# Performance work log

Measured on AMD Instinct MI355X. Metric: run time of the kernel, lower is better.

Reference implementation:

```python
import jax, jax.numpy as jnp
import numpy as np

L, B, F, H, C = 1024, 8, 256, 8, 32  # seq, batch, feature_dim, heads, head_size
EPS = 1e-5


def setup_inputs() -> dict:
    key = jax.random.key(0)
    ks = jax.random.split(key, 12)
    s = 0.02
    f32 = jnp.float32
    return {
        "features": jax.random.normal(ks[0], (L, B, F), f32),
        "ln_g": jnp.ones((F,), f32),
        "ln_b": jnp.zeros((F,), f32),
        "Wq": jax.random.normal(ks[1], (F, H * C), f32) * s,
        "bq": jnp.zeros((H * C,), f32),
        "Wk": jax.random.normal(ks[2], (F, H * C), f32) * s,
        "bk": jnp.zeros((H * C,), f32),
        "Wv": jax.random.normal(ks[3], (F, H * C), f32) * s,
        "bv": jnp.zeros((H * C,), f32),
        "Wb": jax.random.normal(ks[4], (F, H), f32) * s,
        "bb": jnp.zeros((H,), f32),
        "Wg": jax.random.normal(ks[5], (F, H * C), f32) * s,
        "bg": jnp.zeros((H * C,), f32),
        "Wo": jax.random.normal(ks[6], (H * C, F), f32) * s,
        "bo": jnp.zeros((F,), f32),
    }


def _layernorm(x, g, b):
    mu = jnp.mean(x, axis=-1, keepdims=True)
    var = jnp.var(x, axis=-1, keepdims=True)
    return (x - mu) * jax.lax.rsqrt(var + EPS) * g + b


def reference(features, ln_g, ln_b, Wq, bq, Wk, bk, Wv, bv, Wb, bb, Wg, bg, Wo, bo):
    # features: (L, B, F) -- sequence-first layout (see einsum axis analysis)
    x = _layernorm(features, ln_g, ln_b)
    q = (x @ Wq + bq).reshape(L, B, H, C)  # (Lq, B, H, C)
    k = (x @ Wk + bk).reshape(L, B, H, C)  # (Lk, B, H, C)
    v = (x @ Wv + bv).reshape(L, B, H, C)
    bias = x @ Wb + bb                      # (Lk, B, H) per-key-position bias
    gate = jax.nn.sigmoid(x @ Wg + bg).reshape(L, B, H, C)

    sq_c = 1.0 / np.sqrt(C).astype(np.float32)
    # logits[q, b, k, h]
    logits = jnp.einsum('qbhc,kbhc->qbkh', q, k) * sq_c
    logits = logits + jnp.transpose(bias, (1, 0, 2))[None]  # (1, B, Lk, H)
    w = jax.nn.softmax(logits, axis=2)                      # softmax over keys
    attn = jnp.einsum('qbkh,kbhc->qbhc', w, v)              # (Lq, B, H, C)
    out = (attn * gate).reshape(L, B, H * C)
    return out @ Wo + bo                                    # (L, B, F)
```

## Files before the change

kernel.cpp:

```cpp
#include <hip/hip_runtime.h>
#include <math.h>

#define LQ 1024
#define BB 8
#define FF 256
#define HH 8
#define CC 32
#define MROWS (LQ*BB)
static constexpr float EPSV  = 1e-5f;
static constexpr float LOG2E = 1.4426950408889634f;
static constexpr float C1    = 0.17677669529663687f * 1.4426950408889634f;

typedef short  short8  __attribute__((ext_vector_type(8)));
typedef short  short4v __attribute__((ext_vector_type(4)));
typedef float  float4v __attribute__((ext_vector_type(4)));

__device__ inline unsigned short f2bf(float f) {
    unsigned int u = __builtin_bit_cast(unsigned int, f);
    u += 0x7FFFu + ((u >> 16) & 1u);
    return (unsigned short)(u >> 16);
}
__device__ inline float bf2f(unsigned short h) {
    unsigned int u = ((unsigned int)h) << 16;
    return __builtin_bit_cast(float, u);
}
__device__ inline unsigned int cvt_pk_bf16(float a, float b) {
    unsigned int r;
    asm("v_cvt_pk_bf16_f32 %0, %1, %2" : "=v"(r) : "v"(a), "v"(b));
    return r;
}
__device__ __forceinline__ void gl_lds16(const unsigned short* g, unsigned short* l) {
    __builtin_amdgcn_global_load_lds(
        (const __attribute__((address_space(1))) void*)g,
        (__attribute__((address_space(3))) void*)l, 16, 0, 0);
}

__global__ __launch_bounds__(256)
void prep_ln_kernel(const float* __restrict__ x, const float* __restrict__ g,
                    const float* __restrict__ bln,
                    const float* __restrict__ Wq, const float* __restrict__ Wk,
                    const float* __restrict__ Wv, const float* __restrict__ Wg,
                    const float* __restrict__ Wo, const float* __restrict__ Wb,
                    const float* __restrict__ bq, const float* __restrict__ bk,
                    const float* __restrict__ bv, const float* __restrict__ bg,
                    unsigned short* __restrict__ xb, unsigned short* __restrict__ wt,
                    unsigned short* __restrict__ wto,
                    float* __restrict__ bcomb, float* __restrict__ wbt) {
    int bid = blockIdx.x;
    if (bid < 2048) {
        int wid  = threadIdx.x >> 6;
        int lane = threadIdx.x & 63;
        int row  = bid * 4 + wid;
        float4 v = reinterpret_cast<const float4*>(x + (size_t)row * FF)[lane];
        float s  = v.x + v.y + v.z + v.w;
        float sq = v.x*v.x + v.y*v.y + v.z*v.z + v.w*v.w;
        #pragma unroll
        for (int m = 1; m < 64; m <<= 1) {
            s  += __shfl_xor(s,  m);
            sq += __shfl_xor(sq, m);
        }
        float mean = s * (1.0f / FF);
        float var  = sq * (1.0f / FF) - mean * mean;
        float rstd = rsqrtf(var + EPSV);
        float4 gg = reinterpret_cast<const float4*>(g)[lane];
        float4 bv4 = reinterpret_cast<const float4*>(bln)[lane];
        short4v o;
        o[0] = (short)f2bf((v.x - mean) * rstd * gg.x + bv4.x);
        o[1] = (short)f2bf((v.y - mean) * rstd * gg.y + bv4.y);
        o[2] = (short)f2bf((v.z - mean) * rstd * gg.z + bv4.z);
        o[3] = (short)f2bf((v.w - mean) * rstd * gg.w + bv4.w);
        *reinterpret_cast<short4v*>(xb + (size_t)row * FF + lane * 4) = o;
    } else if (bid < 2112) {
        int k0 = (bid - 2048) * 4;
        int nl = threadIdx.x;
        const float* Ws[5] = {Wq, Wk, Wv, Wg, Wo};
        #pragma unroll
        for (int sel = 0; sel < 5; ++sel) {
            const float* W = Ws[sel];
            short4v o;
            #pragma unroll
            for (int j = 0; j < 4; ++j)
                o[j] = (short)f2bf(W[(size_t)(k0 + j) * 256 + nl]);
            unsigned short* dst = (sel < 4)
                ? (wt + ((size_t)sel * 256 + nl) * 256 + k0)
                : (wto + (size_t)nl * 256 + k0);
            *reinterpret_cast<short4v*>(dst) = o;
        }
        if (k0 == 0) {
            bcomb[nl]       = bq[nl];
            bcomb[256 + nl] = bk[nl];
            bcomb[512 + nl] = bv[nl];
            bcomb[768 + nl] = bg[nl];
        }
    } else {
        int nl = threadIdx.x;
        #pragma unroll
        for (int hh = 0; hh < 8; ++hh)
            wbt[hh * 256 + nl] = Wb[(size_t)nl * 8 + hh];
    }
}

__global__ __launch_bounds__(256)
void qkvg_fused_kernel(const unsigned short* __restrict__ A,
                       const unsigned short* __restrict__ Bt,
                       const float* __restrict__ bcomb,
                       const float* __restrict__ wbt,
                       const float* __restrict__ bbv,
                       unsigned short* __restrict__ outq,
                       float* __restrict__ outb) {
    __shared__ unsigned short Asb[128 * 64];
    __shared__ unsigned short Bsb[128 * 64];
    int bid = blockIdx.x;
    int tid = threadIdx.x;

    if (bid >= 512) {
        int idx = (bid - 512) * 256 + tid;
        int row = idx >> 3, hh = idx & 7;
        const unsigned short* xr = A + (size_t)row * 256;
        const float* wr = wbt + hh * 256;
        float s = 0.f;
        #pragma unroll 4
        for (int i = 0; i < 32; ++i) {
            short8 x8 = *reinterpret_cast<const short8*>(xr + i * 8);
            float4 wa = *reinterpret_cast<const float4*>(wr + i * 8);
            float4 wb2 = *reinterpret_cast<const float4*>(wr + i * 8 + 4);
            s += bf2f((unsigned short)x8[0]) * wa.x + bf2f((unsigned short)x8[1]) * wa.y
               + bf2f((unsigned short)x8[2]) * wa.z + bf2f((unsigned short)x8[3]) * wa.w;
            s += bf2f((unsigned short)x8[4]) * wb2.x + bf2f((unsigned short)x8[5]) * wb2.y
               + bf2f((unsigned short)x8[6]) * wb2.z + bf2f((unsigned short)x8[7]) * wb2.w;
        }
        outb[idx] = s + bbv[hh];
        return;
    }

    int lane = tid & 63;
    int w    = tid >> 6;
    int wm   = w >> 1, wn = w & 1;
    int l15  = lane & 15, lg = lane >> 4;
    int bm   = (bid & 63) * 128;
    int bn   = (bid >> 6) * 128;

    float4v acc[4][4];
    #pragma unroll
    for (int i = 0; i < 4; ++i)
        #pragma unroll
        for (int j = 0; j < 4; ++j)
            acc[i][j] = (float4v){0.f, 0.f, 0.f, 0.f};

    for (int k0 = 0; k0 < 256; k0 += 64) {
        __syncthreads();
        #pragma unroll
        for (int j = 0; j < 4; ++j) {
            int c = w * 4 + j;
            int u = c * 64 + lane;
            int row = u >> 3, slot = u & 7;
            size_t gsw = (size_t)row * 256 + k0 + ((slot ^ (row & 7)) * 8);
            gl_lds16(A + (size_t)bm * 256 + gsw, Asb + c * 512);
            gl_lds16(Bt + (size_t)bn * 256 + gsw, Bsb + c * 512);
        }
        __syncthreads();
        #pragma unroll
        for (int kh = 0; kh < 2; ++kh) {
            int slot = kh * 4 + lg;
            short8 af[4], bf[4];
            #pragma unroll
            for (int mf = 0; mf < 4; ++mf) {
                int row = wm * 64 + mf * 16 + l15;
                af[mf] = *reinterpret_cast<const short8*>(
                    Asb + row * 64 + ((slot ^ (row & 7)) * 8));
            }
            #pragma unroll
            for (int nf = 0; nf < 4; ++nf) {
                int row = wn * 64 + nf * 16 + l15;
                bf[nf] = *reinterpret_cast<const short8*>(
                    Bsb + row * 64 + ((slot ^ (row & 7)) * 8));
            }
            #pragma unroll
            for (int mf = 0; mf < 4; ++mf)
                #pragma unroll
                for (int nf = 0; nf < 4; ++nf)
                    acc[mf][nf] = __builtin_amdgcn_mfma_f32_16x16x32_bf16(
                        bf[nf], af[mf], acc[mf][nf], 0, 0, 0);
        }
    }

    int sel = bn >> 8;
    unsigned short* outp = outq + (size_t)sel * MROWS * 256;
    #pragma unroll
    for (int mf = 0; mf < 4; ++mf) {
        int m = bm + wm * 64 + mf * 16 + l15;
        #pragma unroll
        for (int nf = 0; nf < 4; ++nf) {
            int nglob = bn + wn * 64 + nf * 16 + lg * 4;
            float4 b4 = *reinterpret_cast<const float4*>(bcomb + nglob);
            float v0 = acc[mf][nf][0] + b4.x;
            float v1 = acc[mf][nf][1] + b4.y;
            float v2 = acc[mf][nf][2] + b4.z;
            float v3 = acc[mf][nf][3] + b4.w;
            if (sel == 3) {
                v0 = 1.0f / (1.0f + __expf(-v0));
                v1 = 1.0f / (1.0f + __expf(-v1));
                v2 = 1.0f / (1.0f + __expf(-v2));
                v3 = 1.0f / (1.0f + __expf(-v3));
            }
            uint2 st;
            st.x = cvt_pk_bf16(v0, v1);
            st.y = cvt_pk_bf16(v2, v3);
            *reinterpret_cast<uint2*>(outp + (size_t)m * 256 + (nglob & 255)) = st;
        }
    }
}

__global__ __launch_bounds__(256)
void attn_mfma_kernel(const unsigned short* __restrict__ qkvg,
                      const float* __restrict__ biasp,
                      unsigned short* __restrict__ ag) {
    __shared__ unsigned short ksl[128][40];
    __shared__ unsigned short vt[32 * 128];
    __shared__ unsigned short ps[4][32 * 64];
    __shared__ float bias_s[128];
    const unsigned short* qb = qkvg;
    const unsigned short* kb = qkvg + (size_t)MROWS * 256;
    const unsigned short* vb = qkvg + (size_t)MROWS * 256 * 2;
    const unsigned short* gb = qkvg + (size_t)MROWS * 256 * 3;

    int tid  = threadIdx.x;
    int lane = tid & 63;
    int w    = tid >> 6;
    int l15  = lane & 15, lg = lane >> 4;
    int bh   = blockIdx.y;
    int b    = bh >> 3, h = bh & 7;
    int qrow0 = blockIdx.x * 128 + w * 32;

    int cv = (tid & 7) * 4, kp0 = tid >> 3;

    short8 qf[2];
    #pragma unroll
    for (int qt = 0; qt < 2; ++qt)
        qf[qt] = *reinterpret_cast<const short8*>(
            qb + ((size_t)(qrow0 + qt * 16 + l15) * 8 + b) * 256 + h * 32 + lg * 8);

    float lsum[2] = {0.f, 0.f};
    float4v oacc[2][2];
    #pragma unroll
    for (int i = 0; i < 2; ++i)
        #pragma unroll
        for (int j = 0; j < 2; ++j) oacc[i][j] = (float4v){0.f, 0.f, 0.f, 0.f};

    short8 kreg[2]; short4v v0r[2], v1r[2]; float breg = 0.f;
    {
        #pragma unroll
        for (int j = 0; j < 2; ++j) {
            int u = j * 256 + tid;
            int row = u >> 2, slot = u & 3;
            kreg[j] = *reinterpret_cast<const short8*>(
                kb + ((size_t)row * 8 + b) * 256 + h * 32 + slot * 8);
        }
        #pragma unroll
        for (int gI = 0; gI < 2; ++gI) {
            const unsigned short* vp =
                vb + ((size_t)(2 * kp0 + 64 * gI) * 8 + b) * 256 + h * 32 + cv;
            v0r[gI] = *reinterpret_cast<const short4v*>(vp);
            v1r[gI] = *reinterpret_cast<const short4v*>(vp + 8 * 256);
        }
        if (tid < 128) breg = biasp[(size_t)tid * 64 + b * 8 + h] * LOG2E;
    }

    for (int c0 = 0; c0 < LQ; c0 += 128) {
        __syncthreads();
        #pragma unroll
        for (int j = 0; j < 2; ++j) {
            int u = j * 256 + tid;
            int row = u >> 2, slot = u & 3;
            *reinterpret_cast<short8*>(&ksl[row][slot * 8]) = kreg[j];
        }
        #pragma unroll
        for (int gI = 0; gI < 2; ++gI) {
            int kp = kp0 + 32 * gI;
            int slot = kp >> 2;
            #pragma unroll
            for (int j = 0; j < 4; ++j) {
                int c = cv + j;
                unsigned int pk = (unsigned int)(unsigned short)v0r[gI][j] |
                                  ((unsigned int)(unsigned short)v1r[gI][j] << 16);
                int off = c * 128 + ((slot ^ (c & 7)) * 8) + ((2 * kp0) & 7);
                *reinterpret_cast<unsigned int*>(&vt[off]) = pk;
            }
        }
        if (tid < 128) bias_s[tid] = breg;
        __syncthreads();
        int cn = c0 + 128;
        if (cn < LQ) {
            #pragma unroll
            for (int j = 0; j < 2; ++j) {
                int u = j * 256 + tid;
                int row = u >> 2, slot = u & 3;
                kreg[j] = *reinterpret_cast<const short8*>(
                    kb + ((size_t)(cn + row) * 8 + b) * 256 + h * 32 + slot * 8);
            }
            #pragma unroll
            for (int gI = 0; gI < 2; ++gI) {
                const unsigned short* vp =
                    vb + ((size_t)(cn + 2 * kp0 + 64 * gI) * 8 + b) * 256 + h * 32 + cv;
                v0r[gI] = *reinterpret_cast<const short4v*>(vp);
                v1r[gI] = *reinterpret_cast<const short4v*>(vp + 8 * 256);
            }
            if (tid < 128) breg = biasp[(size_t)(cn + tid) * 64 + b * 8 + h] * LOG2E;
        }

        #pragma unroll
        for (int half = 0; half < 2; ++half) {
            __builtin_amdgcn_s_setprio(1);
            float4v sc[2][4];
            #pragma unroll
            for (int kt = 0; kt < 4; ++kt) {
                short8 kf = *reinterpret_cast<const short8*>(
                    &ksl[half * 64 + kt * 16 + l15][lg * 8]);
                #pragma unroll
                for (int qt = 0; qt < 2; ++qt)
                    sc[qt][kt] = __builtin_amdgcn_mfma_f32_16x16x32_bf16(
                        kf, qf[qt], (float4v){0.f, 0.f, 0.f, 0.f}, 0, 0, 0);
            }
            __builtin_amdgcn_s_setprio(0);

            #pragma unroll
            for (int qt = 0; qt < 2; ++qt) {
                int prow = qt * 16 + l15;
                unsigned short* pw = &ps[w][prow * 64];
                int rsw = prow & 7;
                float psum = 0.f;
                #pragma unroll
                for (int kt = 0; kt < 4; ++kt) {
                    float4v b4 = *reinterpret_cast<const float4v*>(
                        &bias_s[half * 64 + kt * 16 + lg * 4]);
                    float p0 = __builtin_amdgcn_exp2f(fmaf(sc[qt][kt][0], C1, b4[0]));
                    float p1 = __builtin_amdgcn_exp2f(fmaf(sc[qt][kt][1], C1, b4[1]));
                    float p2 = __builtin_amdgcn_exp2f(fmaf(sc[qt][kt][2], C1, b4[2]));
                    float p3 = __builtin_amdgcn_exp2f(fmaf(sc[qt][kt][3], C1, b4[3]));
                    psum += (p0 + p1) + (p2 + p3);
                    uint2 pk;
                    pk.x = cvt_pk_bf16(p0, p1);
                    pk.y = cvt_pk_bf16(p2, p3);
                    int slot = kt * 2 + (lg >> 1);
                    *reinterpret_cast<uint2*>(
                        &pw[((slot ^ rsw) * 8) + (lg & 1) * 4]) = pk;
                }
                psum += __shfl_xor(psum, 16);
                psum += __shfl_xor(psum, 32);
                lsum[qt] += psum;
            }

            __builtin_amdgcn_s_setprio(1);
            #pragma unroll
            for (int sub = 0; sub < 2; ++sub) {
                int pslot = sub * 4 + lg;
                int vslot = (half * 2 + sub) * 4 + lg;
                short8 pf[2], vf[2];
                #pragma unroll
                for (int qt = 0; qt < 2; ++qt) {
                    int prow = qt * 16 + l15;
                    pf[qt] = *reinterpret_cast<const short8*>(
                        &ps[w][prow * 64 + ((pslot ^ (prow & 7)) * 8)]);
                }
                #pragma unroll
                for (int ct = 0; ct < 2; ++ct) {
                    int crow = ct * 16 + l15;
                    vf[ct] = *reinterpret_cast<const short8*>(
                        &vt[crow * 128 + ((vslot ^ (crow & 7)) * 8)]);
                }
                #pragma unroll
                for (int qt = 0; qt < 2; ++qt)
                    #pragma unroll
                    for (int ct = 0; ct < 2; ++ct)
                        oacc[qt][ct] = __builtin_amdgcn_mfma_f32_16x16x32_bf16(
                            vf[ct], pf[qt], oacc[qt][ct], 0, 0, 0);
            }
            __builtin_amdgcn_s_setprio(0);
        }
    }

    #pragma unroll
    for (int qt = 0; qt < 2; ++qt) {
        float linv = 1.0f / lsum[qt];
        size_t base = ((size_t)(qrow0 + qt * 16 + l15) * 8 + b) * 256 + h * 32;
        #pragma unroll
        for (int ct = 0; ct < 2; ++ct) {
            int cc0 = ct * 16 + lg * 4;
            short4v g4 = *reinterpret_cast<const short4v*>(gb + base + cc0);
            float v0 = oacc[qt][ct][0] * linv * bf2f((unsigned short)g4[0]);
            float v1 = oacc[qt][ct][1] * linv * bf2f((unsigned short)g4[1]);
            float v2 = oacc[qt][ct][2] * linv * bf2f((unsigned short)g4[2]);
            float v3 = oacc[qt][ct][3] * linv * bf2f((unsigned short)g4[3]);
            uint2 st;
            st.x = cvt_pk_bf16(v0, v1);
            st.y = cvt_pk_bf16(v2, v3);
            *reinterpret_cast<uint2*>(ag + base + cc0) = st;
        }
    }
}

__global__ __launch_bounds__(256)
void gemm_out_kernel(const unsigned short* __restrict__ A,
                     const unsigned short* __restrict__ Bt,
                     const float* __restrict__ bias,
                     float* __restrict__ Cout) {
    __shared__ unsigned short Asb[64 * 64];
    __shared__ unsigned short Bsb[128 * 64];
    int tid  = threadIdx.x;
    int lane = tid & 63;
    int w    = tid >> 6;
    int l15  = lane & 15, lg = lane >> 4;
    int bm   = blockIdx.x * 64;
    int bn   = blockIdx.y * 128;

    float4v acc[4][2];
    #pragma unroll
    for (int i = 0; i < 4; ++i)
        #pragma unroll
        for (int j = 0; j < 2; ++j)
            acc[i][j] = (float4v){0.f, 0.f, 0.f, 0.f};

    for (int k0 = 0; k0 < 256; k0 += 64) {
        __syncthreads();
        #pragma unroll
        for (int j = 0; j < 2; ++j) {
            int c = w * 2 + j;
            int u = c * 64 + lane;
            int row = u >> 3, slot = u & 7;
            gl_lds16(A + (size_t)(bm + row) * 256 + k0 + ((slot ^ (row & 7)) * 8),
                     Asb + c * 512);
        }
        #pragma unroll
        for (int j = 0; j < 4; ++j) {
            int c = w * 4 + j;
            int u = c * 64 + lane;
            int row = u >> 3, slot = u & 7;
            gl_lds16(Bt + (size_t)(bn + row) * 256 + k0 + ((slot ^ (row & 7)) * 8),
                     Bsb + c * 512);
        }
        __syncthreads();
        #pragma unroll
        for (int kh = 0; kh < 2; ++kh) {
            int slot = kh * 4 + lg;
            short8 af[4], bf[2];
            #pragma unroll
            for (int mf = 0; mf < 4; ++mf) {
                int row = mf * 16 + l15;
                af[mf] = *reinterpret_cast<const short8*>(
                    Asb + row * 64 + ((slot ^ (row & 7)) * 8));
            }
            #pragma unroll
            for (int nf = 0; nf < 2; ++nf) {
                int row = w * 32 + nf * 16 + l15;
                bf[nf] = *reinterpret_cast<const short8*>(
                    Bsb + row * 64 + ((slot ^ (row & 7)) * 8));
            }
            #pragma unroll
            for (int mf = 0; mf < 4; ++mf)
                #pragma unroll
                for (int nf = 0; nf < 2; ++nf)
                    acc[mf][nf] = __builtin_amdgcn_mfma_f32_16x16x32_bf16(
                        bf[nf], af[mf], acc[mf][nf], 0, 0, 0);
        }
    }
    #pragma unroll
    for (int mf = 0; mf < 4; ++mf) {
        int m = bm + mf * 16 + l15;
        #pragma unroll
        for (int nf = 0; nf < 2; ++nf) {
            int c0 = bn + w * 32 + nf * 16 + lg * 4;
            float4 b4 = *reinterpret_cast<const float4*>(bias + c0);
            float4 o;
            o.x = acc[mf][nf][0] + b4.x;
            o.y = acc[mf][nf][1] + b4.y;
            o.z = acc[mf][nf][2] + b4.z;
            o.w = acc[mf][nf][3] + b4.w;
            *reinterpret_cast<float4*>(Cout + (size_t)m * 256 + c0) = o;
        }
    }
}

extern "C" void kernel_launch(void* const* d_in, const int* in_sizes, int n_in,
                              void* d_out, int out_size, void* d_ws, size_t ws_size,
                              hipStream_t stream) {
    (void)in_sizes; (void)n_in; (void)out_size; (void)ws_size;
    const float* features = (const float*)d_in[0];
    const float* ln_g = (const float*)d_in[1];
    const float* ln_b = (const float*)d_in[2];
    const float* Wq = (const float*)d_in[3];
    const float* bq = (const float*)d_in[4];
    const float* Wk = (const float*)d_in[5];
    const float* bk = (const float*)d_in[6];
    const float* Wv = (const float*)d_in[7];
    const float* bv = (const float*)d_in[8];
    const float* Wb = (const float*)d_in[9];
    const float* bbv = (const float*)d_in[10];
    const float* Wg = (const float*)d_in[11];
    const float* bg = (const float*)d_in[12];
    const float* Wo = (const float*)d_in[13];
    const float* bo = (const float*)d_in[14];
    float* out = (float*)d_out;

    char* wsb = (char*)d_ws;
    unsigned short* xb    = (unsigned short*)(wsb);
    unsigned short* wt    = (unsigned short*)(wsb + 4194304);
    unsigned short* wto   = (unsigned short*)(wsb + 4718592);
    float*          bcomb = (float*)(wsb + 4849664);
    float*          wbt   = (float*)(wsb + 4853760);
    unsigned short* qkvg  = (unsigned short*)(wsb + 4861952);
    float*          biasb = (float*)(wsb + 21639168);
    unsigned short* agb   = (unsigned short*)(wsb + 21901312);

    prep_ln_kernel<<<dim3(2113), dim3(256), 0, stream>>>(
        features, ln_g, ln_b, Wq, Wk, Wv, Wg, Wo, Wb,
        bq, bk, bv, bg, xb, wt, wto, bcomb, wbt);
    qkvg_fused_kernel<<<dim3(768), dim3(256), 0, stream>>>(
        xb, wt, bcomb, wbt, bbv, qkvg, biasb);
    attn_mfma_kernel<<<dim3(8, 64), dim3(256), 0, stream>>>(
        qkvg, biasb, agb);
    gemm_out_kernel<<<dim3(128, 2), dim3(256), 0, stream>>>(
        agb, wto, bo, out);
}
```

Before: 63.63 us.

## Split attention key tiles across wave pairs and shrink output GEMM N-tile

The attention kernel now runs 512 threads per block. Each pair of waves shares the same 32 query rows and processes one half of each 128-key tile, and the partial output accumulators and row sums are combined through LDS at the end. This doubles the waves per block to hide MFMA and exp latency and removes the serial half loop, at the cost of an extra reduction pass and more LDS. Separately, the output GEMM tile is halved in N (64 instead of 128), doubling the grid to 512 blocks for better CU occupancy with less per-block reuse.

```diff
diff --git a/kernel.cpp b/kernel.cpp
--- a/kernel.cpp
+++ b/kernel.cpp
@@ -211,13 +211,13 @@
     }
 }
 
-__global__ __launch_bounds__(256)
+__global__ __launch_bounds__(512)
 void attn_mfma_kernel(const unsigned short* __restrict__ qkvg,
                       const float* __restrict__ biasp,
                       unsigned short* __restrict__ ag) {
     __shared__ unsigned short ksl[128][40];
     __shared__ unsigned short vt[32 * 128];
-    __shared__ unsigned short ps[4][32 * 64];
+    __shared__ unsigned short ps[8][32 * 64];
     __shared__ float bias_s[128];
     const unsigned short* qb = qkvg;
     const unsigned short* kb = qkvg + (size_t)MROWS * 256;
@@ -230,9 +230,12 @@
     int l15  = lane & 15, lg = lane >> 4;
     int bh   = blockIdx.y;
     int b    = bh >> 3, h = bh & 7;
-    int qrow0 = blockIdx.x * 128 + w * 32;
-
-    int cv = (tid & 7) * 4, kp0 = tid >> 3;
+    int qg   = w >> 1;
+    int kh2  = w & 1;
+    int qrow0 = blockIdx.x * 128 + qg * 32;
+
+    int krow = tid >> 2, kc8 = (tid & 3) * 8;
+    int cv = (tid & 7) * 4, kp = tid >> 3;
 
     short8 qf[2];
     #pragma unroll
@@ -247,154 +250,154 @@
         #pragma unroll
         for (int j = 0; j < 2; ++j) oacc[i][j] = (float4v){0.f, 0.f, 0.f, 0.f};
 
-    short8 kreg[2]; short4v v0r[2], v1r[2]; float breg = 0.f;
+    short8 kreg; short4v v0r, v1r; float breg = 0.f;
     {
-        #pragma unroll
-        for (int j = 0; j < 2; ++j) {
-            int u = j * 256 + tid;
-            int row = u >> 2, slot = u & 3;
-            kreg[j] = *reinterpret_cast<const short8*>(
-                kb + ((size_t)row * 8 + b) * 256 + h * 32 + slot * 8);
-        }
-        #pragma unroll
-        for (int gI = 0; gI < 2; ++gI) {
-            const unsigned short* vp =
-                vb + ((size_t)(2 * kp0 + 64 * gI) * 8 + b) * 256 + h * 32 + cv;
-            v0r[gI] = *reinterpret_cast<const short4v*>(vp);
-            v1r[gI] = *reinterpret_cast<const short4v*>(vp + 8 * 256);
-        }
+        kreg = *reinterpret_cast<const short8*>(
+            kb + ((size_t)krow * 8 + b) * 256 + h * 32 + kc8);
+        const unsigned short* vp =
+            vb + ((size_t)(2 * kp) * 8 + b) * 256 + h * 32 + cv;
+        v0r = *reinterpret_cast<const short4v*>(vp);
+        v1r = *reinterpret_cast<const short4v*>(vp + 8 * 256);
         if (tid < 128) breg = biasp[(size_t)tid * 64 + b * 8 + h] * LOG2E;
     }
 
     for (int c0 = 0; c0 < LQ; c0 += 128) {
         __syncthreads();
-        #pragma unroll
-        for (int j = 0; j < 2; ++j) {
-            int u = j * 256 + tid;
-            int row = u >> 2, slot = u & 3;
-            *reinterpret_cast<short8*>(&ksl[row][slot * 8]) = kreg[j];
-        }
-        #pragma unroll
-        for (int gI = 0; gI < 2; ++gI) {
-            int kp = kp0 + 32 * gI;
+        *reinterpret_cast<short8*>(&ksl[krow][kc8]) = kreg;
+        #pragma unroll
+        for (int j = 0; j < 4; ++j) {
+            int c = cv + j;
+            unsigned int pk = (unsigned int)(unsigned short)v0r[j] |
+                              ((unsigned int)(unsigned short)v1r[j] << 16);
             int slot = kp >> 2;
-            #pragma unroll
-            for (int j = 0; j < 4; ++j) {
-                int c = cv + j;
-                unsigned int pk = (unsigned int)(unsigned short)v0r[gI][j] |
-                                  ((unsigned int)(unsigned short)v1r[gI][j] << 16);
-                int off = c * 128 + ((slot ^ (c & 7)) * 8) + ((2 * kp0) & 7);
-                *reinterpret_cast<unsigned int*>(&vt[off]) = pk;
-            }
+            int off  = c * 128 + ((slot ^ (c & 7)) * 8) + ((2 * kp) & 7);
+            *reinterpret_cast<unsigned int*>(&vt[off]) = pk;
         }
         if (tid < 128) bias_s[tid] = breg;
         __syncthreads();
         int cn = c0 + 128;
         if (cn < LQ) {
-            #pragma unroll
-            for (int j = 0; j < 2; ++j) {
-                int u = j * 256 + tid;
-                int row = u >> 2, slot = u & 3;
-                kreg[j] = *reinterpret_cast<const short8*>(
-                    kb + ((size_t)(cn + row) * 8 + b) * 256 + h * 32 + slot * 8);
-            }
-            #pragma unroll
-            for (int gI = 0; gI < 2; ++gI) {
-                const unsigned short* vp =
-                    vb + ((size_t)(cn + 2 * kp0 + 64 * gI) * 8 + b) * 256 + h * 32 + cv;
-                v0r[gI] = *reinterpret_cast<const short4v*>(vp);
-                v1r[gI] = *reinterpret_cast<const short4v*>(vp + 8 * 256);
-            }
+            kreg = *reinterpret_cast<const short8*>(
+                kb + ((size_t)(cn + krow) * 8 + b) * 256 + h * 32 + kc8);
+            const unsigned short* vp =
+                vb + ((size_t)(cn + 2 * kp) * 8 + b) * 256 + h * 32 + cv;
+            v0r = *reinterpret_cast<const short4v*>(vp);
+            v1r = *reinterpret_cast<const short4v*>(vp + 8 * 256);
             if (tid < 128) breg = biasp[(size_t)(cn + tid) * 64 + b * 8 + h] * LOG2E;
         }
 
-        #pragma unroll
-        for (int half = 0; half < 2; ++half) {
-            __builtin_amdgcn_s_setprio(1);
-            float4v sc[2][4];
+        __builtin_amdgcn_s_setprio(1);
+        float4v sc[2][4];
+        #pragma unroll
+        for (int kt = 0; kt < 4; ++kt) {
+            short8 kf = *reinterpret_cast<const short8*>(
+                &ksl[kh2 * 64 + kt * 16 + l15][lg * 8]);
+            #pragma unroll
+            for (int qt = 0; qt < 2; ++qt)
+                sc[qt][kt] = __builtin_amdgcn_mfma_f32_16x16x32_bf16(
+                    kf, qf[qt], (float4v){0.f, 0.f, 0.f, 0.f}, 0, 0, 0);
+        }
+        __builtin_amdgcn_s_setprio(0);
+
+        #pragma unroll
+        for (int qt = 0; qt < 2; ++qt) {
+            int prow = qt * 16 + l15;
+            unsigned short* pw = &ps[w][prow * 64];
+            int rsw = prow & 7;
+            float psum = 0.f;
             #pragma unroll
             for (int kt = 0; kt < 4; ++kt) {
-                short8 kf = *reinterpret_cast<const short8*>(
-                    &ksl[half * 64 + kt * 16 + l15][lg * 8]);
-                #pragma unroll
-                for (int qt = 0; qt < 2; ++qt)
-                    sc[qt][kt] = __builtin_amdgcn_mfma_f32_16x16x32_bf16(
-                        kf, qf[qt], (float4v){0.f, 0.f, 0.f, 0.f}, 0, 0, 0);
-            }
-            __builtin_amdgcn_s_setprio(0);
-
+                float4v b4 = *reinterpret_cast<const float4v*>(
+                    &bias_s[kh2 * 64 + kt * 16 + lg * 4]);
+                float p0 = __builtin_amdgcn_exp2f(fmaf(sc[qt][kt][0], C1, b4[0]));
+                float p1 = __builtin_amdgcn_exp2f(fmaf(sc[qt][kt][1], C1, b4[1]));
+                float p2 = __builtin_amdgcn_exp2f(fmaf(sc[qt][kt][2], C1, b4[2]));
+                float p3 = __builtin_amdgcn_exp2f(fmaf(sc[qt][kt][3], C1, b4[3]));
+                psum += (p0 + p1) + (p2 + p3);
+                uint2 pk;
+                pk.x = cvt_pk_bf16(p0, p1);
+                pk.y = cvt_pk_bf16(p2, p3);
+                int slot = kt * 2 + (lg >> 1);
+                *reinterpret_cast<uint2*>(
+                    &pw[((slot ^ rsw) * 8) + (lg & 1) * 4]) = pk;
+            }
+            psum += __shfl_xor(psum, 16);
+            psum += __shfl_xor(psum, 32);
+            lsum[qt] += psum;
+        }
+
+        __builtin_amdgcn_s_setprio(1);
+        #pragma unroll
+        for (int kh = 0; kh < 2; ++kh) {
+            int pslot = kh * 4 + lg;
+            int vslot = kh2 * 8 + kh * 4 + lg;
+            short8 pf[2], vf[2];
             #pragma unroll
             for (int qt = 0; qt < 2; ++qt) {
                 int prow = qt * 16 + l15;
-                unsigned short* pw = &ps[w][prow * 64];
-                int rsw = prow & 7;
-                float psum = 0.f;
+                pf[qt] = *reinterpret_cast<const short8*>(
+                    &ps[w][prow * 64 + ((pslot ^ (prow & 7)) * 8)]);
+            }
+            #pragma unroll
+            for (int ct = 0; ct < 2; ++ct) {
+                int crow = ct * 16 + l15;
+                vf[ct] = *reinterpret_cast<const short8*>(
+                    &vt[crow * 128 + ((vslot ^ (crow & 7)) * 8)]);
+            }
+            #pragma unroll
+            for (int qt = 0; qt < 2; ++qt)
                 #pragma unroll
-                for (int kt = 0; kt < 4; ++kt) {
-                    float4v b4 = *reinterpret_cast<const float4v*>(
-                        &bias_s[half * 64 + kt * 16 + lg * 4]);
-                    float p0 = __builtin_amdgcn_exp2f(fmaf(sc[qt][kt][0], C1, b4[0]));
-                    float p1 = __builtin_amdgcn_exp2f(fmaf(sc[qt][kt][1], C1, b4[1]));
-                    float p2 = __builtin_amdgcn_exp2f(fmaf(sc[qt][kt][2], C1, b4[2]));
-                    float p3 = __builtin_amdgcn_exp2f(fmaf(sc[qt][kt][3], C1, b4[3]));
-                    psum += (p0 + p1) + (p2 + p3);
-                    uint2 pk;
-                    pk.x = cvt_pk_bf16(p0, p1);
-                    pk.y = cvt_pk_bf16(p2, p3);
-                    int slot = kt * 2 + (lg >> 1);
-                    *reinterpret_cast<uint2*>(
-                        &pw[((slot ^ rsw) * 8) + (lg & 1) * 4]) = pk;
-                }
-                psum += __shfl_xor(psum, 16);
-                psum += __shfl_xor(psum, 32);
-                lsum[qt] += psum;
-            }
-
-            __builtin_amdgcn_s_setprio(1);
-            #pragma unroll
-            for (int sub = 0; sub < 2; ++sub) {
-                int pslot = sub * 4 + lg;
-                int vslot = (half * 2 + sub) * 4 + lg;
-                short8 pf[2], vf[2];
+                for (int ct = 0; ct < 2; ++ct)
+                    oacc[qt][ct] = __builtin_amdgcn_mfma_f32_16x16x32_bf16(
+                        vf[ct], pf[qt], oacc[qt][ct], 0, 0, 0);
+        }
+        __builtin_amdgcn_s_setprio(0);
+    }
+
+    __syncthreads();
+    float* scr = reinterpret_cast<float*>(&ps[0][0]);
+    if (kh2) {
+        float* dst = scr + ((size_t)(qg * 64 + lane)) * 18;
+        #pragma unroll
+        for (int qt = 0; qt < 2; ++qt)
+            #pragma unroll
+            for (int ct = 0; ct < 2; ++ct)
                 #pragma unroll
-                for (int qt = 0; qt < 2; ++qt) {
-                    int prow = qt * 16 + l15;
-                    pf[qt] = *reinterpret_cast<const short8*>(
-                        &ps[w][prow * 64 + ((pslot ^ (prow & 7)) * 8)]);
-                }
+                for (int r = 0; r < 4; ++r)
+                    dst[(qt * 2 + ct) * 4 + r] = oacc[qt][ct][r];
+        dst[16] = lsum[0];
+        dst[17] = lsum[1];
+    }
+    __syncthreads();
+    if (!kh2) {
+        const float* src = scr + ((size_t)(qg * 64 + lane)) * 18;
+        #pragma unroll
+        for (int qt = 0; qt < 2; ++qt)
+            #pragma unroll
+            for (int ct = 0; ct < 2; ++ct)
                 #pragma unroll
-                for (int ct = 0; ct < 2; ++ct) {
-                    int crow = ct * 16 + l15;
-                    vf[ct] = *reinterpret_cast<const short8*>(
-                        &vt[crow * 128 + ((vslot ^ (crow & 7)) * 8)]);
-                }
-                #pragma unroll
-                for (int qt = 0; qt < 2; ++qt)
-                    #pragma unroll
-                    for (int ct = 0; ct < 2; ++ct)
-                        oacc[qt][ct] = __builtin_amdgcn_mfma_f32_16x16x32_bf16(
-                            vf[ct], pf[qt], oacc[qt][ct], 0, 0, 0);
-            }
-            __builtin_amdgcn_s_setprio(0);
-        }
-    }
-
-    #pragma unroll
-    for (int qt = 0; qt < 2; ++qt) {
-        float linv = 1.0f / lsum[qt];
-        size_t base = ((size_t)(qrow0 + qt * 16 + l15) * 8 + b) * 256 + h * 32;
-        #pragma unroll
-        for (int ct = 0; ct < 2; ++ct) {
-            int cc0 = ct * 16 + lg * 4;
-            short4v g4 = *reinterpret_cast<const short4v*>(gb + base + cc0);
-            float v0 = oacc[qt][ct][0] * linv * bf2f((unsigned short)g4[0]);
-            float v1 = oacc[qt][ct][1] * linv * bf2f((unsigned short)g4[1]);
-            float v2 = oacc[qt][ct][2] * linv * bf2f((unsigned short)g4[2]);
-            float v3 = oacc[qt][ct][3] * linv * bf2f((unsigned short)g4[3]);
-            uint2 st;
-            st.x = cvt_pk_bf16(v0, v1);
-            st.y = cvt_pk_bf16(v2, v3);
-            *reinterpret_cast<uint2*>(ag + base + cc0) = st;
+                for (int r = 0; r < 4; ++r)
+                    oacc[qt][ct][r] += src[(qt * 2 + ct) * 4 + r];
+        lsum[0] += src[16];
+        lsum[1] += src[17];
+
+        #pragma unroll
+        for (int qt = 0; qt < 2; ++qt) {
+            float linv = 1.0f / lsum[qt];
+            size_t base = ((size_t)(qrow0 + qt * 16 + l15) * 8 + b) * 256 + h * 32;
+            #pragma unroll
+            for (int ct = 0; ct < 2; ++ct) {
+                int cc0 = ct * 16 + lg * 4;
+                short4v g4 = *reinterpret_cast<const short4v*>(gb + base + cc0);
+                float v0 = oacc[qt][ct][0] * linv * bf2f((unsigned short)g4[0]);
+                float v1 = oacc[qt][ct][1] * linv * bf2f((unsigned short)g4[1]);
+                float v2 = oacc[qt][ct][2] * linv * bf2f((unsigned short)g4[2]);
+                float v3 = oacc[qt][ct][3] * linv * bf2f((unsigned short)g4[3]);
+                uint2 st;
+                st.x = cvt_pk_bf16(v0, v1);
+                st.y = cvt_pk_bf16(v2, v3);
+                *reinterpret_cast<uint2*>(ag + base + cc0) = st;
+            }
         }
     }
 }
@@ -405,20 +408,17 @@
                      const float* __restrict__ bias,
                      float* __restrict__ Cout) {
     __shared__ unsigned short Asb[64 * 64];
-    __shared__ unsigned short Bsb[128 * 64];
+    __shared__ unsigned short Bsb[64 * 64];
     int tid  = threadIdx.x;
     int lane = tid & 63;
     int w    = tid >> 6;
     int l15  = lane & 15, lg = lane >> 4;
     int bm   = blockIdx.x * 64;
-    int bn   = blockIdx.y * 128;
-
-    float4v acc[4][2];
+    int bn   = blockIdx.y * 64;
+
+    float4v acc[4];
     #pragma unroll
-    for (int i = 0; i < 4; ++i)
-        #pragma unroll
-        for (int j = 0; j < 2; ++j)
-            acc[i][j] = (float4v){0.f, 0.f, 0.f, 0.f};
+    for (int i = 0; i < 4; ++i) acc[i] = (float4v){0.f, 0.f, 0.f, 0.f};
 
     for (int k0 = 0; k0 < 256; k0 += 64) {
         __syncthreads();
@@ -431,8 +431,8 @@
                      Asb + c * 512);
         }
         #pragma unroll
-        for (int j = 0; j < 4; ++j) {
-            int c = w * 4 + j;
+        for (int j = 0; j < 2; ++j) {
+            int c = w * 2 + j;
             int u = c * 64 + lane;
             int row = u >> 3, slot = u & 7;
             gl_lds16(Bt + (size_t)(bn + row) * 256 + k0 + ((slot ^ (row & 7)) * 8),
@@ -442,41 +442,35 @@
         #pragma unroll
         for (int kh = 0; kh < 2; ++kh) {
             int slot = kh * 4 + lg;
-            short8 af[4], bf[2];
+            short8 af[4], bf;
             #pragma unroll
             for (int mf = 0; mf < 4; ++mf) {
                 int row = mf * 16 + l15;
                 af[mf] = *reinterpret_cast<const short8*>(
                     Asb + row * 64 + ((slot ^ (row & 7)) * 8));
             }
-            #pragma unroll
-            for (int nf = 0; nf < 2; ++nf) {
-                int row = w * 32 + nf * 16 + l15;
-                bf[nf] = *reinterpret_cast<const short8*>(
+            {
+                int row = w * 16 + l15;
+                bf = *reinterpret_cast<const short8*>(
                     Bsb + row * 64 + ((slot ^ (row & 7)) * 8));
             }
             #pragma unroll
             for (int mf = 0; mf < 4; ++mf)
-                #pragma unroll
-                for (int nf = 0; nf < 2; ++nf)
-                    acc[mf][nf] = __builtin_amdgcn_mfma_f32_16x16x32_bf16(
-                        bf[nf], af[mf], acc[mf][nf], 0, 0, 0);
-        }
-    }
+                acc[mf] = __builtin_amdgcn_mfma_f32_16x16x32_bf16(
+                    bf, af[mf], acc[mf], 0, 0, 0);
+        }
+    }
+    int c0 = bn + w * 16 + lg * 4;
+    float4 b4 = *reinterpret_cast<const float4*>(bias + c0);
     #pragma unroll
     for (int mf = 0; mf < 4; ++mf) {
         int m = bm + mf * 16 + l15;
-        #pragma unroll
-        for (int nf = 0; nf < 2; ++nf) {
-            int c0 = bn + w * 32 + nf * 16 + lg * 4;
-            float4 b4 = *reinterpret_cast<const float4*>(bias + c0);
-            float4 o;
-            o.x = acc[mf][nf][0] + b4.x;
-            o.y = acc[mf][nf][1] + b4.y;
-            o.z = acc[mf][nf][2] + b4.z;
-            o.w = acc[mf][nf][3] + b4.w;
-            *reinterpret_cast<float4*>(Cout + (size_t)m * 256 + c0) = o;
-        }
+        float4 o;
+        o.x = acc[mf][0] + b4.x;
+        o.y = acc[mf][1] + b4.y;
+        o.z = acc[mf][2] + b4.z;
+        o.w = acc[mf][3] + b4.w;
+        *reinterpret_cast<float4*>(Cout + (size_t)m * 256 + c0) = o;
     }
 }
 
@@ -516,8 +510,8 @@
         bq, bk, bv, bg, xb, wt, wto, bcomb, wbt);
     qkvg_fused_kernel<<<dim3(768), dim3(256), 0, stream>>>(
         xb, wt, bcomb, wbt, bbv, qkvg, biasb);
-    attn_mfma_kernel<<<dim3(8, 64), dim3(256), 0, stream>>>(
+    attn_mfma_kernel<<<dim3(8, 64), dim3(512), 0, stream>>>(
         qkvg, biasb, agb);
-    gemm_out_kernel<<<dim3(128, 2), dim3(256), 0, stream>>>(
+    gemm_out_kernel<<<dim3(128, 4), dim3(256), 0, stream>>>(
         agb, wto, bo, out);
 }
```

After: 58.49 us, median of 2. 1.09x faster.
